# Performance work log

Measured on AMD Instinct MI355X. Metric: run time of the kernel, lower is better.

Reference implementation:

```python
import jax, jax.numpy as jnp
import numpy as np

THR = 1.0  # snntorch Leaky default threshold

# Heaviside spike with ATan surrogate gradient (snntorch surrogate.atan, alpha=2)
@jax.custom_vjp
def atan_spike(x):
    return (x > 0).astype(x.dtype)

def _spike_fwd(x):
    return atan_spike(x), x

def _spike_bwd(x, g):
    # d/dx of surrogate: (alpha/2) / (1 + (pi/2*alpha*x)^2) with alpha=2 -> 1/(1+(pi*x)^2)
    return (g / (1.0 + (jnp.pi * x) ** 2),)

atan_spike.defvjp(_spike_fwd, _spike_bwd)


def setup_inputs() -> dict:
    key = jax.random.key(0)
    ks = jax.random.split(key, 5)
    B, T = 256, 100
    D, H, O = 34 * 34 * 2, 1000, 10
    data = jax.random.normal(ks[0], (B, T, 2, 34, 34), jnp.float32)
    lim1 = 1.0 / np.sqrt(D)
    lim2 = 1.0 / np.sqrt(H)
    w1 = jax.random.uniform(ks[1], (H, D), jnp.float32, -lim1, lim1)
    b1 = jax.random.uniform(ks[2], (H,), jnp.float32, -lim1, lim1)
    w2 = jax.random.uniform(ks[3], (O, H), jnp.float32, -lim2, lim2)
    b2 = jax.random.uniform(ks[4], (O,), jnp.float32, -lim2, lim2)
    beta = jnp.float32(0.9)
    return {"data": data, "w1": w1, "b1": b1, "w2": w2, "b2": b2, "beta": beta}


def reference(data, w1, b1, w2, b2, beta):
    B, T = data.shape[0], data.shape[1]
    H, O = w1.shape[0], w2.shape[0]
    x = data.reshape(B, T, -1).transpose(1, 0, 2)  # [T, B, D] (Flatten per step)
    # Input currents to layer 1 are state-independent: one batched GEMM.
    cur1_all = jnp.einsum('tbd,hd->tbh', x, w1) + b1  # [T, B, H]

    mem1 = jnp.zeros((B, H), data.dtype)
    spk1 = jnp.zeros((B, H), data.dtype)
    mem2 = jnp.zeros((B, O), data.dtype)
    spk2 = jnp.zeros((B, O), data.dtype)

    def step(carry, cur1):
        mem1, spk1, mem2, spk2 = carry
        # snntorch Leaky, reset_mechanism='subtract':
        # mem = beta*mem + input - reset*threshold ; spk = fire(mem)
        mem1 = beta * mem1 + cur1 - spk1 * THR
        spk1 = atan_spike(mem1 - THR)
        cur2 = spk1 @ w2.T + b2
        mem2 = beta * mem2 + cur2 - spk2 * THR
        spk2 = atan_spike(mem2 - THR)
        return (mem1, spk1, mem2, spk2), (spk2, mem2)

    _, (spk_rec, mem_rec) = jax.lax.scan(step, (mem1, spk1, mem2, spk2), cur1_all)
    return spk_rec, mem_rec  # each [T, B, 10]
```

## Files before the change

### kernel.cpp

```cpp
#include <hip/hip_runtime.h>
#include <hip/hip_bf16.h>
#include <stdint.h>

#define T_STEPS 100
#define B_SZ    256
#define D_IN    2312
#define H_SZ    1000
#define O_SZ    10
#define M_ROWS  (B_SZ * T_STEPS)
#define K_PAD   2336
#define KT      73
#define W_ROWS  1024

#define A_SCALE   16.0f
#define W_SCALE   64.0f
#define INV_SCALE (1.0f / 1024.0f)

typedef __attribute__((ext_vector_type(4))) float     floatx4;
typedef __attribute__((ext_vector_type(8))) _Float16  halfx8;

#define ASYNC_COPY16(g, l)                                             \
  __builtin_amdgcn_global_load_lds(                                    \
      (const __attribute__((address_space(1))) void*)(g),              \
      (__attribute__((address_space(3))) void*)(l), 16, 0, 0)

__global__ __launch_bounds__(256)
void splitW_kernel(const float* __restrict__ W,
                   _Float16* __restrict__ wHi,
                   _Float16* __restrict__ wLo)
{
  const int r = blockIdx.x;
  const bool rvalid = (r < H_SZ);
  const float* w = W + (size_t)(rvalid ? r : 0) * D_IN;
  _Float16* ho = wHi + (size_t)r * K_PAD;
  _Float16* lo = wLo + (size_t)r * K_PAD;
  for (int c = threadIdx.x; c < K_PAD / 8; c += 256) {
    const int k0 = c * 8;
    const bool v = rvalid && (k0 + 8 <= D_IN);
    _Float16 h[8], l[8];
    #pragma unroll
    for (int e = 0; e < 8; ++e) {
      const float x = v ? w[k0 + e] * W_SCALE : 0.f;
      const _Float16 hb = (_Float16)x;
      h[e] = hb;
      l[e] = (_Float16)(x - (float)hb);
    }
    *reinterpret_cast<uint4*>(ho + k0) = *reinterpret_cast<const uint4*>(h);
    *reinterpret_cast<uint4*>(lo + k0) = *reinterpret_cast<const uint4*>(l);
  }
}

__global__ __launch_bounds__(256)
void gemm1_fused(const float* __restrict__ A,
                 const _Float16* __restrict__ wHi,
                 const _Float16* __restrict__ wLo,
                 const float* __restrict__ b1,
                 float* __restrict__ C)
{
  __shared__ _Float16 sAh[128 * 32];
  __shared__ _Float16 sAl[128 * 32];
  __shared__ _Float16 sBh[128 * 32];
  __shared__ _Float16 sBl[128 * 32];

  const int tid  = threadIdx.x;
  const int n0   = blockIdx.x * 128;
  const int m0   = blockIdx.y * 128;
  const int wid  = tid >> 6;
  const int lane = tid & 63;
  const int wm   = (wid & 1) * 64;
  const int wn   = (wid >> 1) * 64;
  const int quad = lane >> 4;
  const int l16  = lane & 15;

  floatx4 acc[4][4];
  #pragma unroll
  for (int i = 0; i < 4; ++i)
    #pragma unroll
    for (int j = 0; j < 4; ++j)
      acc[i][j] = floatx4{0.f, 0.f, 0.f, 0.f};

  const int r0  = tid >> 2;
  const int r1  = r0 + 64;
  const int sl  = tid & 3;
  const int rho = (r0 >> 1) & 3;
  const int ko  = ((sl ^ rho) * 8);

  const float* gA0 = A + (size_t)(m0 + r0) * D_IN + ko;
  const float* gA1 = A + (size_t)(m0 + r1) * D_IN + ko;
  const _Float16* gBh0 = wHi + (size_t)(n0 + r0) * K_PAD + ko;
  const _Float16* gBh1 = wHi + (size_t)(n0 + r1) * K_PAD + ko;
  const _Float16* gBl0 = wLo + (size_t)(n0 + r0) * K_PAD + ko;
  const _Float16* gBl1 = wLo + (size_t)(n0 + r1) * K_PAD + ko;

  _Float16* lAh0 = sAh + (size_t)tid * 8;
  _Float16* lAh1 = sAh + (size_t)(tid + 256) * 8;
  _Float16* lAl0 = sAl + (size_t)tid * 8;
  _Float16* lAl1 = sAl + (size_t)(tid + 256) * 8;
  _Float16* lBh0 = sBh + (size_t)tid * 8;
  _Float16* lBh1 = sBh + (size_t)(tid + 256) * 8;
  _Float16* lBl0 = sBl + (size_t)tid * 8;
  _Float16* lBl1 = sBl + (size_t)(tid + 256) * 8;

  const int fo = (quad ^ ((l16 >> 1) & 3)) * 8;

  float a0[8], a1[8];
  *reinterpret_cast<float4*>(a0)     = *reinterpret_cast<const float4*>(gA0);
  *reinterpret_cast<float4*>(a0 + 4) = *reinterpret_cast<const float4*>(gA0 + 4);
  *reinterpret_cast<float4*>(a1)     = *reinterpret_cast<const float4*>(gA1);
  *reinterpret_cast<float4*>(a1 + 4) = *reinterpret_cast<const float4*>(gA1 + 4);

  for (int kt = 0; kt < KT; ++kt) {
    const int koff = kt * 32;
    __syncthreads();
    ASYNC_COPY16(gBh0 + koff, lBh0);
    ASYNC_COPY16(gBh1 + koff, lBh1);
    ASYNC_COPY16(gBl0 + koff, lBl0);
    ASYNC_COPY16(gBl1 + koff, lBl1);

    {
      _Float16 h0[8], l0[8], h1[8], l1[8];
      #pragma unroll
      for (int e = 0; e < 8; ++e) {
        const float v0 = a0[e] * A_SCALE;
        const _Float16 hb0 = (_Float16)v0;
        h0[e] = hb0; l0[e] = (_Float16)(v0 - (float)hb0);
        const float v1 = a1[e] * A_SCALE;
        const _Float16 hb1 = (_Float16)v1;
        h1[e] = hb1; l1[e] = (_Float16)(v1 - (float)hb1);
      }
      *reinterpret_cast<uint4*>(lAh0) = *reinterpret_cast<const uint4*>(h0);
      *reinterpret_cast<uint4*>(lAl0) = *reinterpret_cast<const uint4*>(l0);
      *reinterpret_cast<uint4*>(lAh1) = *reinterpret_cast<const uint4*>(h1);
      *reinterpret_cast<uint4*>(lAl1) = *reinterpret_cast<const uint4*>(l1);
    }
    __syncthreads();

    if (kt + 1 < KT) {
      const int k = (kt + 1) * 32 + ko;
      if (k < D_IN) {
        *reinterpret_cast<float4*>(a0)     = *reinterpret_cast<const float4*>(gA0 + (kt + 1) * 32);
        *reinterpret_cast<float4*>(a0 + 4) = *reinterpret_cast<const float4*>(gA0 + (kt + 1) * 32 + 4);
        *reinterpret_cast<float4*>(a1)     = *reinterpret_cast<const float4*>(gA1 + (kt + 1) * 32);
        *reinterpret_cast<float4*>(a1 + 4) = *reinterpret_cast<const float4*>(gA1 + (kt + 1) * 32 + 4);
      } else {
        #pragma unroll
        for (int e = 0; e < 8; ++e) { a0[e] = 0.f; a1[e] = 0.f; }
      }
    }

    halfx8 ah[4], bh[4], al[4], bl[4];
    #pragma unroll
    for (int i = 0; i < 4; ++i) {
      const int row = (wm + i * 16 + l16) * 32 + fo;
      ah[i] = *reinterpret_cast<const halfx8*>(sAh + row);
      al[i] = *reinterpret_cast<const halfx8*>(sAl + row);
    }
    #pragma unroll
    for (int j = 0; j < 4; ++j) {
      const int row = (wn + j * 16 + l16) * 32 + fo;
      bh[j] = *reinterpret_cast<const halfx8*>(sBh + row);
      bl[j] = *reinterpret_cast<const halfx8*>(sBl + row);
    }
    #pragma unroll
    for (int i = 0; i < 4; ++i)
      #pragma unroll
      for (int j = 0; j < 4; ++j)
        acc[i][j] = __builtin_amdgcn_mfma_f32_16x16x32_f16(ah[i], bh[j], acc[i][j], 0, 0, 0);
    #pragma unroll
    for (int i = 0; i < 4; ++i)
      #pragma unroll
      for (int j = 0; j < 4; ++j)
        acc[i][j] = __builtin_amdgcn_mfma_f32_16x16x32_f16(al[i], bh[j], acc[i][j], 0, 0, 0);
    #pragma unroll
    for (int i = 0; i < 4; ++i)
      #pragma unroll
      for (int j = 0; j < 4; ++j)
        acc[i][j] = __builtin_amdgcn_mfma_f32_16x16x32_f16(ah[i], bl[j], acc[i][j], 0, 0, 0);
  }

  #pragma unroll
  for (int j = 0; j < 4; ++j) {
    const int col = n0 + wn + j * 16 + l16;
    if (col < H_SZ) {
      const float bias = b1[col];
      #pragma unroll
      for (int i = 0; i < 4; ++i) {
        const int row = m0 + wm + i * 16 + quad * 4;
        #pragma unroll
        for (int r = 0; r < 4; ++r)
          C[(size_t)(row + r) * H_SZ + col] = acc[i][j][r] * INV_SCALE + bias;
      }
    }
  }
}

__global__ __launch_bounds__(256)
void scan1_kernel(const float* __restrict__ cur1,
                  const float* __restrict__ beta_p,
                  __hip_bfloat16* __restrict__ spk1)
{
  const int h = blockIdx.x * 256 + threadIdx.x;
  const int b = blockIdx.y;
  if (h >= H_SZ) return;
  const float beta = beta_p[0];
  const float* c    = cur1 + (size_t)b * T_STEPS * H_SZ + h;
  __hip_bfloat16* s = spk1 + (size_t)b * T_STEPS * H_SZ + h;
  float mem = 0.f, spk = 0.f;
  #pragma unroll 4
  for (int t = 0; t < T_STEPS; ++t) {
    mem = beta * mem + c[(size_t)t * H_SZ] - spk;
    spk = (mem > 1.0f) ? 1.0f : 0.0f;
    s[(size_t)t * H_SZ] = __float2bfloat16(spk);
  }
}

__global__ __launch_bounds__(256)
void gemm2_kernel(const __hip_bfloat16* __restrict__ spk1,
                  const float* __restrict__ w2,
                  float* __restrict__ cur2)
{
  const int wid  = threadIdx.x >> 6;
  const int lane = threadIdx.x & 63;
  const int m    = blockIdx.x * 4 + wid;

  float acc[O_SZ];
  #pragma unroll
  for (int o = 0; o < O_SZ; ++o) acc[o] = 0.f;

  const __hip_bfloat16* row = spk1 + (size_t)m * H_SZ;
  #pragma unroll
  for (int it = 0; it < 16; ++it) {
    const int h = it * 64 + lane;
    if (h < H_SZ) {
      const float s = __bfloat162float(row[h]);
      if (s != 0.f) {
        #pragma unroll
        for (int o = 0; o < O_SZ; ++o)
          acc[o] += w2[o * H_SZ + h];
      }
    }
  }
  #pragma unroll
  for (int o = 0; o < O_SZ; ++o) {
    float v = acc[o];
    #pragma unroll
    for (int off = 32; off > 0; off >>= 1) v += __shfl_down(v, off);
    if (lane == 0) cur2[(size_t)m * O_SZ + o] = v;
  }
}

__global__ __launch_bounds__(256)
void scan2_kernel(const float* __restrict__ cur2,
                  const float* __restrict__ b2,
                  const float* __restrict__ beta_p,
                  float* __restrict__ out)
{
  const int idx = blockIdx.x * 256 + threadIdx.x;
  if (idx >= B_SZ * O_SZ) return;
  const int b = idx / O_SZ;
  const int o = idx % O_SZ;
  const float beta = beta_p[0];
  const float bias = b2[o];
  float* spk_rec = out;
  float* mem_rec = out + (size_t)T_STEPS * B_SZ * O_SZ;
  float mem = 0.f, spk = 0.f;
  for (int t = 0; t < T_STEPS; ++t) {
    const float cur = cur2[((size_t)b * T_STEPS + t) * O_SZ + o] + bias;
    mem = beta * mem + cur - spk;
    spk = (mem > 1.0f) ? 1.0f : 0.0f;
    const size_t oi = ((size_t)t * B_SZ + b) * O_SZ + o;
    spk_rec[oi] = spk;
    mem_rec[oi] = mem;
  }
}

extern "C" void kernel_launch(void* const* d_in, const int* in_sizes, int n_in,
                              void* d_out, int out_size, void* d_ws, size_t ws_size,
                              hipStream_t stream)
{
  const float* data = (const float*)d_in[0];
  const float* w1   = (const float*)d_in[1];
  const float* b1   = (const float*)d_in[2];
  const float* w2   = (const float*)d_in[3];
  const float* b2   = (const float*)d_in[4];
  const float* beta = (const float*)d_in[5];
  float* out = (float*)d_out;

  char* p = (char*)d_ws;
  auto take = [&](size_t n) { char* q = p; p += (n + 255) & ~(size_t)255; return q; };
  _Float16*       wHi  = (_Float16*)take((size_t)W_ROWS * K_PAD * 2);
  _Float16*       wLo  = (_Float16*)take((size_t)W_ROWS * K_PAD * 2);
  float*          cur1 = (float*)take((size_t)M_ROWS * H_SZ * 4);
  __hip_bfloat16* spk1 = (__hip_bfloat16*)take((size_t)M_ROWS * H_SZ * 2);
  float*          cur2 = (float*)take((size_t)M_ROWS * O_SZ * 4);

  splitW_kernel<<<dim3(W_ROWS), 256, 0, stream>>>(w1, wHi, wLo);
  gemm1_fused<<<dim3(8, M_ROWS / 128), 256, 0, stream>>>(data, wHi, wLo, b1, cur1);
  scan1_kernel<<<dim3(4, B_SZ), 256, 0, stream>>>(cur1, beta, spk1);
  gemm2_kernel<<<dim3(M_ROWS / 4), 256, 0, stream>>>(spk1, w2, cur2);
  scan2_kernel<<<dim3(10), 256, 0, stream>>>(cur2, b2, beta, out);
}
```

Before: 888.3 us.

## Double-buffer weight tiles in GEMM1 and remap blocks for XCD-aware tile order

The GEMM1 kernel now keeps two LDS buffers for the weight hi/lo tiles and issues the async copy for the next K-step before computing the current one, with explicit s_waitcnt and raw barriers in place of the two __syncthreads per iteration. The A loads are made branch-free by clamping the offset and masking with a validity flag. The grid becomes 1D with a block-id remap, so the blocks of each M-tile group land on the same XCD and can share weight and activation data in L2. This trades extra LDS and hand-managed wait counts, which could be wrong, for more overlap of memory traffic with MFMA work.

```diff
diff --git a/kernel.cpp b/kernel.cpp
--- a/kernel.cpp
+++ b/kernel.cpp
@@ -59,12 +59,18 @@
 {
   __shared__ _Float16 sAh[128 * 32];
   __shared__ _Float16 sAl[128 * 32];
-  __shared__ _Float16 sBh[128 * 32];
-  __shared__ _Float16 sBl[128 * 32];
+  __shared__ _Float16 sBh[2][128 * 32];
+  __shared__ _Float16 sBl[2][128 * 32];
 
   const int tid  = threadIdx.x;
-  const int n0   = blockIdx.x * 128;
-  const int m0   = blockIdx.y * 128;
+
+  const int id  = blockIdx.x;
+  const int j   = id >> 3;
+  const int mt  = (id & 7) * 25 + (j >> 3);
+  const int nt  = j & 7;
+  const int m0  = mt * 128;
+  const int n0  = nt * 128;
+
   const int wid  = tid >> 6;
   const int lane = tid & 63;
   const int wm   = (wid & 1) * 64;
@@ -76,8 +82,8 @@
   #pragma unroll
   for (int i = 0; i < 4; ++i)
     #pragma unroll
-    for (int j = 0; j < 4; ++j)
-      acc[i][j] = floatx4{0.f, 0.f, 0.f, 0.f};
+    for (int jj = 0; jj < 4; ++jj)
+      acc[i][jj] = floatx4{0.f, 0.f, 0.f, 0.f};
 
   const int r0  = tid >> 2;
   const int r1  = r0 + 64;
@@ -96,10 +102,8 @@
   _Float16* lAh1 = sAh + (size_t)(tid + 256) * 8;
   _Float16* lAl0 = sAl + (size_t)tid * 8;
   _Float16* lAl1 = sAl + (size_t)(tid + 256) * 8;
-  _Float16* lBh0 = sBh + (size_t)tid * 8;
-  _Float16* lBh1 = sBh + (size_t)(tid + 256) * 8;
-  _Float16* lBl0 = sBl + (size_t)tid * 8;
-  _Float16* lBl1 = sBl + (size_t)(tid + 256) * 8;
+  const int lb0 = tid * 8;
+  const int lb1 = (tid + 256) * 8;
 
   const int fo = (quad ^ ((l16 >> 1) & 3)) * 8;
 
@@ -108,23 +112,24 @@
   *reinterpret_cast<float4*>(a0 + 4) = *reinterpret_cast<const float4*>(gA0 + 4);
   *reinterpret_cast<float4*>(a1)     = *reinterpret_cast<const float4*>(gA1);
   *reinterpret_cast<float4*>(a1 + 4) = *reinterpret_cast<const float4*>(gA1 + 4);
+  bool curValid = true;
+
+  ASYNC_COPY16(gBh0, &sBh[0][lb0]);
+  ASYNC_COPY16(gBh1, &sBh[0][lb1]);
+  ASYNC_COPY16(gBl0, &sBl[0][lb0]);
+  ASYNC_COPY16(gBl1, &sBl[0][lb1]);
 
   for (int kt = 0; kt < KT; ++kt) {
-    const int koff = kt * 32;
-    __syncthreads();
-    ASYNC_COPY16(gBh0 + koff, lBh0);
-    ASYNC_COPY16(gBh1 + koff, lBh1);
-    ASYNC_COPY16(gBl0 + koff, lBl0);
-    ASYNC_COPY16(gBl1 + koff, lBl1);
+    const int p = kt & 1;
 
     {
       _Float16 h0[8], l0[8], h1[8], l1[8];
       #pragma unroll
       for (int e = 0; e < 8; ++e) {
-        const float v0 = a0[e] * A_SCALE;
+        const float v0 = curValid ? a0[e] * A_SCALE : 0.f;
         const _Float16 hb0 = (_Float16)v0;
         h0[e] = hb0; l0[e] = (_Float16)(v0 - (float)hb0);
-        const float v1 = a1[e] * A_SCALE;
+        const float v1 = curValid ? a1[e] * A_SCALE : 0.f;
         const _Float16 hb1 = (_Float16)v1;
         h1[e] = hb1; l1[e] = (_Float16)(v1 - (float)hb1);
       }
@@ -133,20 +138,26 @@
       *reinterpret_cast<uint4*>(lAh1) = *reinterpret_cast<const uint4*>(h1);
       *reinterpret_cast<uint4*>(lAl1) = *reinterpret_cast<const uint4*>(l1);
     }
-    __syncthreads();
 
     if (kt + 1 < KT) {
-      const int k = (kt + 1) * 32 + ko;
-      if (k < D_IN) {
-        *reinterpret_cast<float4*>(a0)     = *reinterpret_cast<const float4*>(gA0 + (kt + 1) * 32);
-        *reinterpret_cast<float4*>(a0 + 4) = *reinterpret_cast<const float4*>(gA0 + (kt + 1) * 32 + 4);
-        *reinterpret_cast<float4*>(a1)     = *reinterpret_cast<const float4*>(gA1 + (kt + 1) * 32);
-        *reinterpret_cast<float4*>(a1 + 4) = *reinterpret_cast<const float4*>(gA1 + (kt + 1) * 32 + 4);
-      } else {
-        #pragma unroll
-        for (int e = 0; e < 8; ++e) { a0[e] = 0.f; a1[e] = 0.f; }
-      }
-    }
+      const int kb = (kt + 1) * 32;
+      const bool v = (kb + ko) < D_IN;
+      const int off = v ? kb : 0;
+      *reinterpret_cast<float4*>(a0)     = *reinterpret_cast<const float4*>(gA0 + off);
+      *reinterpret_cast<float4*>(a0 + 4) = *reinterpret_cast<const float4*>(gA0 + off + 4);
+      *reinterpret_cast<float4*>(a1)     = *reinterpret_cast<const float4*>(gA1 + off);
+      *reinterpret_cast<float4*>(a1 + 4) = *reinterpret_cast<const float4*>(gA1 + off + 4);
+      curValid = v;
+      ASYNC_COPY16(gBh0 + kb, &sBh[p ^ 1][lb0]);
+      ASYNC_COPY16(gBh1 + kb, &sBh[p ^ 1][lb1]);
+      ASYNC_COPY16(gBl0 + kb, &sBl[p ^ 1][lb0]);
+      ASYNC_COPY16(gBl1 + kb, &sBl[p ^ 1][lb1]);
+      asm volatile("s_waitcnt vmcnt(8) lgkmcnt(0)" ::: "memory");
+    } else {
+      asm volatile("s_waitcnt vmcnt(0) lgkmcnt(0)" ::: "memory");
+    }
+    __builtin_amdgcn_s_barrier();
+    asm volatile("" ::: "memory");
 
     halfx8 ah[4], bh[4], al[4], bl[4];
     #pragma unroll
@@ -156,31 +167,35 @@
       al[i] = *reinterpret_cast<const halfx8*>(sAl + row);
     }
     #pragma unroll
-    for (int j = 0; j < 4; ++j) {
-      const int row = (wn + j * 16 + l16) * 32 + fo;
-      bh[j] = *reinterpret_cast<const halfx8*>(sBh + row);
-      bl[j] = *reinterpret_cast<const halfx8*>(sBl + row);
+    for (int jj = 0; jj < 4; ++jj) {
+      const int row = (wn + jj * 16 + l16) * 32 + fo;
+      bh[jj] = *reinterpret_cast<const halfx8*>(&sBh[p][row]);
+      bl[jj] = *reinterpret_cast<const halfx8*>(&sBl[p][row]);
     }
     #pragma unroll
     for (int i = 0; i < 4; ++i)
       #pragma unroll
-      for (int j = 0; j < 4; ++j)
-        acc[i][j] = __builtin_amdgcn_mfma_f32_16x16x32_f16(ah[i], bh[j], acc[i][j], 0, 0, 0);
+      for (int jj = 0; jj < 4; ++jj)
+        acc[i][jj] = __builtin_amdgcn_mfma_f32_16x16x32_f16(ah[i], bh[jj], acc[i][jj], 0, 0, 0);
     #pragma unroll
     for (int i = 0; i < 4; ++i)
       #pragma unroll
-      for (int j = 0; j < 4; ++j)
-        acc[i][j] = __builtin_amdgcn_mfma_f32_16x16x32_f16(al[i], bh[j], acc[i][j], 0, 0, 0);
+      for (int jj = 0; jj < 4; ++jj)
+        acc[i][jj] = __builtin_amdgcn_mfma_f32_16x16x32_f16(al[i], bh[jj], acc[i][jj], 0, 0, 0);
     #pragma unroll
     for (int i = 0; i < 4; ++i)
       #pragma unroll
-      for (int j = 0; j < 4; ++j)
-        acc[i][j] = __builtin_amdgcn_mfma_f32_16x16x32_f16(ah[i], bl[j], acc[i][j], 0, 0, 0);
-  }
-
-  #pragma unroll
-  for (int j = 0; j < 4; ++j) {
-    const int col = n0 + wn + j * 16 + l16;
+      for (int jj = 0; jj < 4; ++jj)
+        acc[i][jj] = __builtin_amdgcn_mfma_f32_16x16x32_f16(ah[i], bl[jj], acc[i][jj], 0, 0, 0);
+
+    asm volatile("" ::: "memory");
+    __builtin_amdgcn_s_barrier();
+    asm volatile("" ::: "memory");
+  }
+
+  #pragma unroll
+  for (int jj = 0; jj < 4; ++jj) {
+    const int col = n0 + wn + jj * 16 + l16;
     if (col < H_SZ) {
       const float bias = b1[col];
       #pragma unroll
@@ -188,7 +203,7 @@
         const int row = m0 + wm + i * 16 + quad * 4;
         #pragma unroll
         for (int r = 0; r < 4; ++r)
-          C[(size_t)(row + r) * H_SZ + col] = acc[i][j][r] * INV_SCALE + bias;
+          C[(size_t)(row + r) * H_SZ + col] = acc[i][jj][r] * INV_SCALE + bias;
       }
     }
   }
@@ -295,7 +310,7 @@
   float*          cur2 = (float*)take((size_t)M_ROWS * O_SZ * 4);
 
   splitW_kernel<<<dim3(W_ROWS), 256, 0, stream>>>(w1, wHi, wLo);
-  gemm1_fused<<<dim3(8, M_ROWS / 128), 256, 0, stream>>>(data, wHi, wLo, b1, cur1);
+  gemm1_fused<<<dim3(1600), 256, 0, stream>>>(data, wHi, wLo, b1, cur1);
   scan1_kernel<<<dim3(4, B_SZ), 256, 0, stream>>>(cur1, beta, spk1);
   gemm2_kernel<<<dim3(M_ROWS / 4), 256, 0, stream>>>(spk1, w2, cur2);
   scan2_kernel<<<dim3(10), 256, 0, stream>>>(cur2, b2, beta, out);
```

Result: slower. 911.9 us (+2.7%).
